# Kernel tuning notes

Hardware: AMD Instinct MI355X
Metric: run time of the kernel (lower is better)

The kernel has to match this reference:

```python
import jax, jax.numpy as jnp
import numpy as np

EPS = 1e-7
MAX_TANH = 1.0 - 1e-6  # clamp for arctanh stability


def _norm(v):
    # last-axis L2 norm, clamped away from zero
    return jnp.maximum(jnp.linalg.norm(v, axis=-1, keepdims=True), EPS)


def log_map_zero(y):
    # Poincare ball (c=1) log map at the origin
    n = _norm(y)
    return jnp.arctanh(jnp.clip(n, 0.0, MAX_TANH)) * y / n


def exp_map_zero(v):
    # Poincare ball (c=1) exp map at the origin
    n = _norm(v)
    return jnp.tanh(n) * v / n


def h_add(x, y):
    # Mobius addition x (+) y on the Poincare ball (c=1)
    xy = jnp.sum(x * y, axis=-1, keepdims=True)
    x2 = jnp.sum(x * x, axis=-1, keepdims=True)
    y2 = jnp.sum(y * y, axis=-1, keepdims=True)
    num = (1.0 + 2.0 * xy + y2) * x + (1.0 - x2) * y
    den = 1.0 + 2.0 * xy + x2 * y2
    return num / jnp.maximum(den, EPS)


def h_mul(x, W):
    # Mobius matrix-vector multiply: exp0( log0(x) @ W )
    return exp_map_zero(log_map_zero(x) @ W)


def setup_inputs() -> dict:
    key = jax.random.key(0)
    k1, k2, k3, k4 = jax.random.split(key, 4)
    N, F_IN, F_OUT = 8192, 128, 128
    # node features inside the unit ball: ||x|| ~ 0.05*sqrt(128) ~ 0.57
    x = 0.05 * jax.random.normal(k1, (N, F_IN), dtype=jnp.float32)
    # sparse-ish row-normalized dense adjacency
    a = (jax.random.uniform(k2, (N, N)) < 0.01).astype(jnp.float32)
    adj = a / jnp.maximum(a.sum(axis=1, keepdims=True), 1.0)
    # xavier-uniform-ish weights
    lim_e = np.sqrt(6.0 / (F_IN + F_IN)) * np.sqrt(2.0)
    lim_l = np.sqrt(6.0 / (2 * F_IN + F_OUT)) * np.sqrt(2.0)
    embed = jax.random.uniform(k3, (F_IN, F_IN), minval=-lim_e, maxval=lim_e, dtype=jnp.float32)
    layer = jax.random.uniform(k4, (2 * F_IN, F_OUT), minval=-lim_l, maxval=lim_l, dtype=jnp.float32)
    embed_bias = jnp.zeros((F_IN,), dtype=jnp.float32)
    layer_bias = jnp.zeros((F_OUT,), dtype=jnp.float32)
    return {"x": x, "adj": adj, "embed": embed, "layer": layer,
            "embed_bias": embed_bias, "layer_bias": layer_bias}


def reference(x, adj, embed, layer, embed_bias, layer_bias):
    # h = (embed (x)mobius x) (+) embed_bias
    h = h_mul(x, embed)                      # [N, F_IN]
    h = h_add(h, embed_bias[None, :])
    # neighbor aggregation in tangent space at origin
    neigh = exp_map_zero(adj @ log_map_zero(h))   # [N, F_IN]
    # out = (layer (x)mobius [x ; neigh]) (+) layer_bias
    out = h_mul(jnp.concatenate((x, neigh), axis=1), layer)  # [N, F_OUT]
    out = h_add(out, layer_bias[None, :])
    return out
```

## Files before the change

kernel.cpp:

```cpp
#include <hip/hip_runtime.h>
#include <math.h>

#define EPS  1e-7f
#define MAXT 0.999999f

typedef short  s16x8  __attribute__((ext_vector_type(8)));
typedef float  f32x16 __attribute__((ext_vector_type(16)));

__device__ __forceinline__ float waveRedSum(float v) {
    #pragma unroll
    for (int off = 32; off > 0; off >>= 1)
        v += __shfl_xor(v, off, 64);
    return v;
}

__device__ __forceinline__ unsigned short f2bf(float f) {
    unsigned u = __float_as_uint(f);
    u += 0x7fff + ((u >> 16) & 1);
    return (unsigned short)(u >> 16);
}

__global__ __launch_bounds__(256) void kA(const float* __restrict__ x,
                                          const float* __restrict__ embed,
                                          const float* __restrict__ ebias,
                                          unsigned short* __restrict__ vpack) {
    __shared__ float u[4][128];
    const int wave = threadIdx.x >> 6;
    const int lane = threadIdx.x & 63;
    const int row  = blockIdx.x * 4 + wave;
    const int c0   = lane * 2;

    const float2 xr = *(const float2*)(x + (size_t)row * 128 + c0);

    float n2 = waveRedSum(xr.x * xr.x + xr.y * xr.y);
    float n  = fmaxf(sqrtf(n2), EPS);
    float sc = atanhf(fminf(n, MAXT)) / n;
    u[wave][c0]     = xr.x * sc;
    u[wave][c0 + 1] = xr.y * sc;
    __syncthreads();

    float a0 = 0.f, a1 = 0.f;
    #pragma unroll 8
    for (int k = 0; k < 128; k++) {
        float  uk = u[wave][k];
        float2 e  = *(const float2*)(embed + (size_t)k * 128 + c0);
        a0 = fmaf(uk, e.x, a0);
        a1 = fmaf(uk, e.y, a1);
    }

    float np2 = waveRedSum(a0 * a0 + a1 * a1);
    float np  = fmaxf(sqrtf(np2), EPS);
    float se  = tanhf(np) / np;
    float h0 = a0 * se, h1 = a1 * se;
    float x2 = np2 * se * se;

    float bx = ebias[c0], by = ebias[c0 + 1];
    float xy = waveRedSum(h0 * bx + h1 * by);
    float y2 = waveRedSum(bx * bx + by * by);
    float den = fmaxf(1.f + 2.f * xy + x2 * y2, EPS);
    float cx = 1.f + 2.f * xy + y2;
    float cy = 1.f - x2;
    float hb0 = (cx * h0 + cy * bx) / den;
    float hb1 = (cx * h1 + cy * by) / den;

    float m2 = waveRedSum(hb0 * hb0 + hb1 * hb1);
    float m  = fmaxf(sqrtf(m2), EPS);
    float sl = atanhf(fminf(m, MAXT)) / m;
    float v0 = hb0 * sl, v1 = hb1 * sl;

    const int tbase = (row >> 4) * 2048 + (row & 15);
    vpack[tbase + c0 * 16]       = f2bf(v0);
    vpack[tbase + (c0 + 1) * 16] = f2bf(v1);
}

#define BK 128

__global__ __launch_bounds__(256) void kB(const float* __restrict__ adj,
                                          const unsigned short* __restrict__ vpack,
                                          float* __restrict__ t) {
    __shared__ __align__(16) unsigned short As[32][BK + 8];

    const int tid  = threadIdx.x;
    const int wave = tid >> 6;
    const int lane = tid & 63;
    const int r0   = blockIdx.x * 32;

    const int srow = tid >> 3;
    const int scol = (tid & 7) * 16;
    const float* aptr = adj + (size_t)(r0 + srow) * 8192 + scol;

    const int m  = lane & 31;
    const int kh = lane >> 5;
    const int n  = wave * 32 + m;
    const unsigned short* vb = vpack + (size_t)n * 16 + kh * 8;

    f32x16 acc = {0.f};

    float4 f0 = *(const float4*)(aptr + 0);
    float4 f1 = *(const float4*)(aptr + 4);
    float4 f2 = *(const float4*)(aptr + 8);
    float4 f3 = *(const float4*)(aptr + 12);

    for (int kc = 0; kc < 8192; kc += BK) {
        __syncthreads();

        union { unsigned short u[8]; s16x8 v; } p0, p1;
        p0.u[0] = f2bf(f0.x); p0.u[1] = f2bf(f0.y); p0.u[2] = f2bf(f0.z); p0.u[3] = f2bf(f0.w);
        p0.u[4] = f2bf(f1.x); p0.u[5] = f2bf(f1.y); p0.u[6] = f2bf(f1.z); p0.u[7] = f2bf(f1.w);
        p1.u[0] = f2bf(f2.x); p1.u[1] = f2bf(f2.y); p1.u[2] = f2bf(f2.z); p1.u[3] = f2bf(f2.w);
        p1.u[4] = f2bf(f3.x); p1.u[5] = f2bf(f3.y); p1.u[6] = f2bf(f3.z); p1.u[7] = f2bf(f3.w);
        *(s16x8*)&As[srow][scol]     = p0.v;
        *(s16x8*)&As[srow][scol + 8] = p1.v;
        __syncthreads();

        if (kc + BK < 8192) {
            aptr += BK;
            f0 = *(const float4*)(aptr + 0);
            f1 = *(const float4*)(aptr + 4);
            f2 = *(const float4*)(aptr + 8);
            f3 = *(const float4*)(aptr + 12);
        }

        const int ktile0 = kc >> 4;
        #pragma unroll
        for (int kk = 0; kk < BK / 16; kk++) {
            s16x8 a = *(const s16x8*)&As[m][kk * 16 + kh * 8];
            s16x8 b = *(const s16x8*)(vb + (size_t)(ktile0 + kk) * 2048);
            acc = __builtin_amdgcn_mfma_f32_32x32x16_bf16(a, b, acc, 0, 0, 0);
        }
    }

    #pragma unroll
    for (int r = 0; r < 16; r++) {
        int row = r0 + (r & 3) + 8 * (r >> 2) + 4 * kh;
        t[(size_t)row * 128 + n] = acc[r];
    }
}

__global__ __launch_bounds__(256) void kC(const float* __restrict__ x,
                                          const float* __restrict__ t,
                                          const float* __restrict__ layer,
                                          const float* __restrict__ lbias,
                                          float* __restrict__ out) {
    __shared__ float w[4][256];
    const int wave = threadIdx.x >> 6;
    const int lane = threadIdx.x & 63;
    const int row  = blockIdx.x * 4 + wave;
    const int c0   = lane * 2;

    const float2 tr = *(const float2*)(t + (size_t)row * 128 + c0);
    const float2 xr = *(const float2*)(x + (size_t)row * 128 + c0);

    float st = waveRedSum(tr.x * tr.x + tr.y * tr.y);
    float sx = waveRedSum(xr.x * xr.x + xr.y * xr.y);

    float nt = fmaxf(sqrtf(st), EPS);
    float se = tanhf(nt) / nt;

    float ncat2 = sx + st * se * se;
    float ncat  = fmaxf(sqrtf(ncat2), EPS);
    float sw    = atanhf(fminf(ncat, MAXT)) / ncat;
    w[wave][c0]           = xr.x * sw;
    w[wave][c0 + 1]       = xr.y * sw;
    w[wave][128 + c0]     = tr.x * se * sw;
    w[wave][128 + c0 + 1] = tr.y * se * sw;
    __syncthreads();

    float a0 = 0.f, a1 = 0.f;
    #pragma unroll 8
    for (int k = 0; k < 256; k++) {
        float  wk = w[wave][k];
        float2 e  = *(const float2*)(layer + (size_t)k * 128 + c0);
        a0 = fmaf(wk, e.x, a0);
        a1 = fmaf(wk, e.y, a1);
    }

    float np2 = waveRedSum(a0 * a0 + a1 * a1);
    float np  = fmaxf(sqrtf(np2), EPS);
    float so  = tanhf(np) / np;
    float o0 = a0 * so, o1 = a1 * so;
    float x2 = np2 * so * so;

    float bx = lbias[c0], by = lbias[c0 + 1];
    float xy = waveRedSum(o0 * bx + o1 * by);
    float y2 = waveRedSum(bx * bx + by * by);
    float den = fmaxf(1.f + 2.f * xy + x2 * y2, EPS);
    float cx = 1.f + 2.f * xy + y2;
    float cy = 1.f - x2;

    float2 res;
    res.x = (cx * o0 + cy * bx) / den;
    res.y = (cx * o1 + cy * by) / den;
    *(float2*)(out + (size_t)row * 128 + c0) = res;
}

extern "C" void kernel_launch(void* const* d_in, const int* in_sizes, int n_in,
                              void* d_out, int out_size, void* d_ws, size_t ws_size,
                              hipStream_t stream) {
    const float* x     = (const float*)d_in[0];
    const float* adj   = (const float*)d_in[1];
    const float* embed = (const float*)d_in[2];
    const float* layer = (const float*)d_in[3];
    const float* eb    = (const float*)d_in[4];
    const float* lb    = (const float*)d_in[5];
    float* out = (float*)d_out;

    unsigned short* vpack = (unsigned short*)d_ws;
    float* t = (float*)((char*)d_ws + 8192 * 128 * sizeof(unsigned short));

    kA<<<2048, 256, 0, stream>>>(x, embed, eb, vpack);
    kB<<<256,  256, 0, stream>>>(adj, vpack, t);
    kC<<<2048, 256, 0, stream>>>(x, t, layer, lb, out);
}
```

Baseline: 532.3 us.

## Split-K the adjacency GEMM across blocks and reduce partials in final kernel

The dense adj @ v kernel previously launched only 256 blocks, each walking the full 8192-long K dimension. It now splits K into up to 8 slices along blockIdx.y, with the slice count chosen from available workspace. Each slice writes its own fp32 partial result, and the final kernel sums the partials before its epilogue. This is meant to fill more of the GPU's compute units during the bandwidth-bound 256MB adjacency read, at the cost of extra partial-result writes and reads.

```diff
diff --git a/kernel.cpp b/kernel.cpp
--- a/kernel.cpp
+++ b/kernel.cpp
@@ -77,17 +77,20 @@
 
 __global__ __launch_bounds__(256) void kB(const float* __restrict__ adj,
                                           const unsigned short* __restrict__ vpack,
-                                          float* __restrict__ t) {
+                                          float* __restrict__ tpart,
+                                          int klen) {
     __shared__ __align__(16) unsigned short As[32][BK + 8];
 
     const int tid  = threadIdx.x;
     const int wave = tid >> 6;
     const int lane = tid & 63;
     const int r0   = blockIdx.x * 32;
+    const int k0   = blockIdx.y * klen;
+    float* tout    = tpart + (size_t)blockIdx.y * 8192 * 128;
 
     const int srow = tid >> 3;
     const int scol = (tid & 7) * 16;
-    const float* aptr = adj + (size_t)(r0 + srow) * 8192 + scol;
+    const float* aptr = adj + (size_t)(r0 + srow) * 8192 + k0 + scol;
 
     const int m  = lane & 31;
     const int kh = lane >> 5;
@@ -101,7 +104,8 @@
     float4 f2 = *(const float4*)(aptr + 8);
     float4 f3 = *(const float4*)(aptr + 12);
 
-    for (int kc = 0; kc < 8192; kc += BK) {
+    const int kiters = klen / BK;
+    for (int it = 0; it < kiters; it++) {
         __syncthreads();
 
         union { unsigned short u[8]; s16x8 v; } p0, p1;
@@ -113,7 +117,7 @@
         *(s16x8*)&As[srow][scol + 8] = p1.v;
         __syncthreads();
 
-        if (kc + BK < 8192) {
+        if (it + 1 < kiters) {
             aptr += BK;
             f0 = *(const float4*)(aptr + 0);
             f1 = *(const float4*)(aptr + 4);
@@ -121,7 +125,7 @@
             f3 = *(const float4*)(aptr + 12);
         }
 
-        const int ktile0 = kc >> 4;
+        const int ktile0 = (k0 + it * BK) >> 4;
         #pragma unroll
         for (int kk = 0; kk < BK / 16; kk++) {
             s16x8 a = *(const s16x8*)&As[m][kk * 16 + kh * 8];
@@ -133,22 +137,27 @@
     #pragma unroll
     for (int r = 0; r < 16; r++) {
         int row = r0 + (r & 3) + 8 * (r >> 2) + 4 * kh;
-        t[(size_t)row * 128 + n] = acc[r];
+        tout[(size_t)row * 128 + n] = acc[r];
     }
 }
 
 __global__ __launch_bounds__(256) void kC(const float* __restrict__ x,
-                                          const float* __restrict__ t,
+                                          const float* __restrict__ tpart,
                                           const float* __restrict__ layer,
                                           const float* __restrict__ lbias,
-                                          float* __restrict__ out) {
+                                          float* __restrict__ out,
+                                          int S) {
     __shared__ float w[4][256];
     const int wave = threadIdx.x >> 6;
     const int lane = threadIdx.x & 63;
     const int row  = blockIdx.x * 4 + wave;
     const int c0   = lane * 2;
 
-    const float2 tr = *(const float2*)(t + (size_t)row * 128 + c0);
+    float2 tr = *(const float2*)(tpart + (size_t)row * 128 + c0);
+    for (int s = 1; s < S; s++) {
+        float2 p = *(const float2*)(tpart + (size_t)s * 8192 * 128 + (size_t)row * 128 + c0);
+        tr.x += p.x; tr.y += p.y;
+    }
     const float2 xr = *(const float2*)(x + (size_t)row * 128 + c0);
 
     float st = waveRedSum(tr.x * tr.x + tr.y * tr.y);
@@ -205,10 +214,18 @@
     const float* lb    = (const float*)d_in[5];
     float* out = (float*)d_out;
 
+    const size_t vbytes = (size_t)8192 * 128 * 2;
+    const size_t slice  = (size_t)8192 * 128 * 4;
+
+    int S = 1;
+    if      (ws_size >= vbytes + 8 * slice) S = 8;
+    else if (ws_size >= vbytes + 4 * slice) S = 4;
+    else if (ws_size >= vbytes + 2 * slice) S = 2;
+
     unsigned short* vpack = (unsigned short*)d_ws;
-    float* t = (float*)((char*)d_ws + 8192 * 128 * sizeof(unsigned short));
+    float* tpart = (float*)((char*)d_ws + vbytes);
 
     kA<<<2048, 256, 0, stream>>>(x, embed, eb, vpack);
-    kB<<<256,  256, 0, stream>>>(adj, vpack, t);
-    kC<<<2048, 256, 0, stream>>>(x, t, layer, lb, out);
-}
+    kB<<<dim3(256, S), 256, 0, stream>>>(adj, vpack, tpart, 8192 / S);
+    kC<<<2048, 256, 0, stream>>>(x, tpart, layer, lb, out, S);
+}
```

New measurement: 499.3 us. 6.2% less time.
